# Optimization experiments

Measured on AMD Instinct MI355X. Metric: run time of the kernel, lower is better.

Reference implementation:

```python
import jax, jax.numpy as jnp
import numpy as np

M = 4096          # output features (n_rows, c_3)
H = 4096          # input features  (n_cols, c_4)
NNZ_PER_ROW = 2048
NNZ = M * NNZ_PER_ROW
B, S = 4, 2048    # batch, seq -> flattened to N = B*S row-vecs in the original loop


def setup_inputs() -> dict:
    key = jax.random.key(0)
    k1, k2, k3 = jax.random.split(key, 3)
    x = jax.random.normal(k1, (B, S, H), jnp.float32)
    values = jax.random.normal(k2, (NNZ,), jnp.float32) * 0.02
    # unique, sorted column indices per row (valid CSR structure)
    scores = jax.random.uniform(k3, (M, H))
    cols = jnp.argsort(scores, axis=1)[:, :NNZ_PER_ROW].astype(jnp.int32)
    col_idx = jnp.sort(cols, axis=1).reshape(-1)
    row_ptr = (jnp.arange(M + 1, dtype=jnp.int32) * NNZ_PER_ROW)
    return {"x": x, "values": values, "col_idx": col_idx, "row_ptr": row_ptr}


def _decode_csr(values, col_idx, row_ptr, n_rows, n_cols):
    """Decode compressed (CSR) weight once into dense [n_rows, n_cols]."""
    nnz = values.shape[0]
    row_ids = jnp.searchsorted(row_ptr, jnp.arange(nnz, dtype=row_ptr.dtype), side='right') - 1
    W = jnp.zeros((n_rows, n_cols), values.dtype).at[row_ids, col_idx].add(values)
    return W


def reference(x, values, col_idx, row_ptr):
    # Original loops macko_spmv.multiply over each flattened row of x:
    #   out_flat[i] = W_sparse @ x_flat[i]
    # Fused/batched equivalent: decode the compressed weight once, single GEMM.
    W = _decode_csr(values, col_idx, row_ptr, M, H)     # [M, H]
    out = jnp.einsum('bsh,mh->bsm', x, W)               # [B, S, M]
    return out
```

## Files before the change

### kernel.cpp

```cpp
#include <hip/hip_runtime.h>
#include <hip/hip_bf16.h>

#define H_DIM   4096
#define M_DIM   4096
#define N_ROWS  8192
#define NNZ_ROW 2048

typedef __bf16 bf16x8 __attribute__((ext_vector_type(8)));
typedef float  f32x4  __attribute__((ext_vector_type(4)));

__device__ __forceinline__ unsigned short f2bf(float f) {
    unsigned int u = __float_as_uint(f);
    u += 0x7fffu + ((u >> 16) & 1u);
    return (unsigned short)(u >> 16);
}

__device__ __forceinline__ void gld_lds16(const void* g, void* l) {
    __builtin_amdgcn_global_load_lds(
        (__attribute__((address_space(1))) const void*)g,
        (__attribute__((address_space(3))) void*)l,
        16, 0, 0);
}

__global__ __launch_bounds__(256) void decode_w_frag_kernel(
        const float* __restrict__ values,
        const int*   __restrict__ col_idx,
        unsigned short* __restrict__ Wf) {
    __shared__ unsigned short buf[4 * H_DIM];
    const int r4 = blockIdx.x;
    const int t  = threadIdx.x;

    uint4 z = make_uint4(0u, 0u, 0u, 0u);
    #pragma unroll
    for (int i = 0; i < 8; ++i) ((uint4*)buf)[i * 256 + t] = z;
    __syncthreads();

    #pragma unroll
    for (int rl = 0; rl < 4; ++rl) {
        const long base = ((long)(4 * r4 + rl)) * NNZ_ROW;
        #pragma unroll
        for (int j = 0; j < NNZ_ROW; j += 256) {
            float v = values[base + j + t];
            int   c = col_idx[base + j + t];
            buf[rl * H_DIM + c] = f2bf(v);
        }
    }
    __syncthreads();

    const int ct  = r4 >> 2;
    const int fr0 = (r4 & 3) * 4;
    #pragma unroll
    for (int it = 0; it < 8; ++it) {
        const int task = it * 256 + t;
        const int rl = task & 3;
        const int jq = (task >> 2) & 3;
        const int kc = task >> 4;
        uint4 v = *(const uint4*)&buf[rl * H_DIM + kc * 32 + jq * 8];
        const long dst = (((long)ct * 128 + kc) * 64 + jq * 16 + fr0 + rl) * 8;
        *(uint4*)&Wf[dst] = v;
    }
}

__global__ __launch_bounds__(256) void convert_x_kernel(
        const float4* __restrict__ x, uint4* __restrict__ xb) {
    const long i = blockIdx.x * 256L + threadIdx.x;
    float4 a = x[2 * i];
    float4 b = x[2 * i + 1];
    union { unsigned short s[8]; uint4 v; } r;
    r.s[0] = f2bf(a.x); r.s[1] = f2bf(a.y); r.s[2] = f2bf(a.z); r.s[3] = f2bf(a.w);
    r.s[4] = f2bf(b.x); r.s[5] = f2bf(b.y); r.s[6] = f2bf(b.z); r.s[7] = f2bf(b.w);
    xb[i] = r.v;
}

__global__ __launch_bounds__(256) void gemm_flatb_kernel(
        const unsigned short* __restrict__ A,
        const unsigned short* __restrict__ Bf,
        float* __restrict__ C) {
    __shared__ unsigned short As[128 * 32];

    const int t    = threadIdx.x;
    const int lane = t & 63;
    const int wid  = t >> 6;
    const int wm   = wid >> 1;
    const int wn   = wid & 1;

    const int gid   = blockIdx.x;
    const int ctile = (gid & 7) * 4 + ((gid >> 3) & 3);
    const int rtile = gid >> 5;
    const long row0 = (long)rtile * 128;
    const long col0 = (long)ctile * 128;

    const int ar = t >> 2;
    const int q  = t & 3;
    const unsigned short* Ag0 = A + (row0 + ar) * H_DIM + ((q ^ (ar & 3)) * 8);
    const unsigned short* Ag1 = Ag0 + 64L * H_DIM;
    unsigned short* Al0 = &As[t * 8];
    unsigned short* Al1 = &As[t * 8 + 2048];

    const uint4* Bbase = (const uint4*)Bf +
        ((long)(ctile * 8 + wn * 4) * 128) * 64 + lane;

    f32x4 acc[4][4];
    #pragma unroll
    for (int i = 0; i < 4; ++i)
        #pragma unroll
        for (int j = 0; j < 4; ++j)
            acc[i][j] = (f32x4)0.0f;

    const int fr = lane & 15;
    const int jq = lane >> 4;
    const int achunk = (jq ^ (fr & 3)) * 8;

    for (int kc = 0; kc < H_DIM / 32; ++kc) {
        __syncthreads();
        gld_lds16(Ag0 + kc * 32, Al0);
        gld_lds16(Ag1 + kc * 32, Al1);

        union { uint4 u; bf16x8 v; } b[4];
        #pragma unroll
        for (int j = 0; j < 4; ++j)
            b[j].u = Bbase[(long)kc * 64 + j * 128 * 64];

        __syncthreads();

        bf16x8 a[4];
        #pragma unroll
        for (int i = 0; i < 4; ++i) {
            const int r = wm * 64 + i * 16 + fr;
            a[i] = *(const bf16x8*)&As[r * 32 + achunk];
        }

        #pragma unroll
        for (int i = 0; i < 4; ++i)
            #pragma unroll
            for (int j = 0; j < 4; ++j)
                acc[i][j] = __builtin_amdgcn_mfma_f32_16x16x32_bf16(
                                a[i], b[j].v, acc[i][j], 0, 0, 0);
    }

    const int dcol = lane & 15;
    const int drow = (lane >> 4) * 4;
    #pragma unroll
    for (int i = 0; i < 4; ++i) {
        const long r = row0 + wm * 64 + i * 16 + drow;
        #pragma unroll
        for (int j = 0; j < 4; ++j) {
            float* cp = C + r * M_DIM + (col0 + wn * 64 + j * 16 + dcol);
            #pragma unroll
            for (int qq = 0; qq < 4; ++qq)
                cp[qq * (long)M_DIM] = acc[i][j][qq];
        }
    }
}

__global__ __launch_bounds__(256) void naive_kernel(
        const float* __restrict__ x, const float* __restrict__ vals,
        const int* __restrict__ cols, float* __restrict__ out) {
    const long idx = blockIdx.x * 256L + threadIdx.x;
    const int  m   = (int)(idx & (M_DIM - 1));
    const long n   = idx >> 12;
    const float* xr = x + n * H_DIM;
    const float* v  = vals + (long)m * NNZ_ROW;
    const int*   c  = cols + (long)m * NNZ_ROW;
    float s = 0.f;
    for (int j = 0; j < NNZ_ROW; ++j) s += v[j] * xr[c[j]];
    out[idx] = s;
}

extern "C" void kernel_launch(void* const* d_in, const int* in_sizes, int n_in,
                              void* d_out, int out_size, void* d_ws, size_t ws_size,
                              hipStream_t stream) {
    const float* x       = (const float*)d_in[0];
    const float* values  = (const float*)d_in[1];
    const int*   col_idx = (const int*)d_in[2];
    float* out = (float*)d_out;

    const size_t wbytes = (size_t)M_DIM * H_DIM * sizeof(unsigned short);
    const size_t xbytes = (size_t)N_ROWS * H_DIM * sizeof(unsigned short);

    if (ws_size >= wbytes + xbytes) {
        unsigned short* Wf = (unsigned short*)d_ws;
        unsigned short* Xb = (unsigned short*)((char*)d_ws + wbytes);

        decode_w_frag_kernel<<<M_DIM / 4, 256, 0, stream>>>(values, col_idx, Wf);

        const long xvec = (long)N_ROWS * H_DIM / 8;
        convert_x_kernel<<<(int)(xvec / 256), 256, 0, stream>>>(
            (const float4*)x, (uint4*)Xb);

        gemm_flatb_kernel<<<(N_ROWS / 128) * (M_DIM / 128), 256, 0, stream>>>(
            Xb, Wf, out);
    } else {
        naive_kernel<<<(int)((long)N_ROWS * M_DIM / 256), 256, 0, stream>>>(
            x, values, col_idx, out);
    }
}
```

Baseline: 616.3 us.

## Replace GEMM with 256x256 double-buffered LDS-tiled kernel and row-major W

The GEMM moves from 128x128 tiles, where B fragments come straight from global memory in a pre-shuffled layout, to 256x256 tiles with 8 waves. Both A and B are staged into double-buffered, XOR-swizzled LDS with global_load_lds, and explicit vmcnt/lgkmcnt waits, sched barriers and setprio interleave the loads with MFMA work. The W decode now writes plain row-major bf16, and the x conversion becomes a grid-stride loop. The aim is more data reuse per tile and hiding memory latency behind compute, at the cost of much more LDS per block (128 KB) and hand-tuned waitcnt logic that is fragile.

Result: faster. 499.5 us (-19.0%).

```diff
diff --git a/kernel.cpp b/kernel.cpp
--- a/kernel.cpp
+++ b/kernel.cpp
@@ -1,10 +1,10 @@
 #include <hip/hip_runtime.h>
-#include <hip/hip_bf16.h>
 
 #define H_DIM   4096
 #define M_DIM   4096
 #define N_ROWS  8192
 #define NNZ_ROW 2048
+#define NT      (H_DIM / 64)
 
 typedef __bf16 bf16x8 __attribute__((ext_vector_type(8)));
 typedef float  f32x4  __attribute__((ext_vector_type(4)));
@@ -22,10 +22,23 @@
         16, 0, 0);
 }
 
-__global__ __launch_bounds__(256) void decode_w_frag_kernel(
+__device__ __forceinline__ void wg_barrier() {
+    __builtin_amdgcn_sched_barrier(0);
+    asm volatile("" ::: "memory");
+    __builtin_amdgcn_s_barrier();
+    asm volatile("" ::: "memory");
+    __builtin_amdgcn_sched_barrier(0);
+}
+
+#define LGKM0_FENCE() do { \
+    asm volatile("s_waitcnt lgkmcnt(0)" ::: "memory"); \
+    __builtin_amdgcn_sched_barrier(0); \
+} while (0)
+
+__global__ __launch_bounds__(256) void decode_w_kernel(
         const float* __restrict__ values,
         const int*   __restrict__ col_idx,
-        unsigned short* __restrict__ Wf) {
+        unsigned short* __restrict__ W) {
     __shared__ unsigned short buf[4 * H_DIM];
     const int r4 = blockIdx.x;
     const int t  = threadIdx.x;
@@ -47,109 +60,188 @@
     }
     __syncthreads();
 
-    const int ct  = r4 >> 2;
-    const int fr0 = (r4 & 3) * 4;
+    const long wbase = (long)(4 * r4) * H_DIM;
     #pragma unroll
     for (int it = 0; it < 8; ++it) {
-        const int task = it * 256 + t;
-        const int rl = task & 3;
-        const int jq = (task >> 2) & 3;
-        const int kc = task >> 4;
-        uint4 v = *(const uint4*)&buf[rl * H_DIM + kc * 32 + jq * 8];
-        const long dst = (((long)ct * 128 + kc) * 64 + jq * 16 + fr0 + rl) * 8;
-        *(uint4*)&Wf[dst] = v;
+        const int s = it * 256 + t;
+        *(uint4*)&W[wbase + (long)s * 8] = *(const uint4*)&buf[s * 8];
     }
 }
 
 __global__ __launch_bounds__(256) void convert_x_kernel(
-        const float4* __restrict__ x, uint4* __restrict__ xb) {
-    const long i = blockIdx.x * 256L + threadIdx.x;
-    float4 a = x[2 * i];
-    float4 b = x[2 * i + 1];
-    union { unsigned short s[8]; uint4 v; } r;
-    r.s[0] = f2bf(a.x); r.s[1] = f2bf(a.y); r.s[2] = f2bf(a.z); r.s[3] = f2bf(a.w);
-    r.s[4] = f2bf(b.x); r.s[5] = f2bf(b.y); r.s[6] = f2bf(b.z); r.s[7] = f2bf(b.w);
-    xb[i] = r.v;
-}
-
-__global__ __launch_bounds__(256) void gemm_flatb_kernel(
+        const float4* __restrict__ x, unsigned long long* __restrict__ xb) {
+    const long total = (long)N_ROWS * H_DIM / 4;
+    for (long i = (long)blockIdx.x * 256 + threadIdx.x; i < total;
+         i += (long)gridDim.x * 256) {
+        float4 a = x[i];
+        union { unsigned short s[4]; unsigned long long v; } r;
+        r.s[0] = f2bf(a.x); r.s[1] = f2bf(a.y);
+        r.s[2] = f2bf(a.z); r.s[3] = f2bf(a.w);
+        xb[i] = r.v;
+    }
+}
+
+__global__ __launch_bounds__(512, 2) void gemm256_kernel(
         const unsigned short* __restrict__ A,
-        const unsigned short* __restrict__ Bf,
+        const unsigned short* __restrict__ B,
         float* __restrict__ C) {
-    __shared__ unsigned short As[128 * 32];
+    __shared__ unsigned short lds[2 * 32768];
 
     const int t    = threadIdx.x;
     const int lane = t & 63;
     const int wid  = t >> 6;
-    const int wm   = wid >> 1;
-    const int wn   = wid & 1;
-
-    const int gid   = blockIdx.x;
-    const int ctile = (gid & 7) * 4 + ((gid >> 3) & 3);
-    const int rtile = gid >> 5;
-    const long row0 = (long)rtile * 128;
-    const long col0 = (long)ctile * 128;
-
-    const int ar = t >> 2;
-    const int q  = t & 3;
-    const unsigned short* Ag0 = A + (row0 + ar) * H_DIM + ((q ^ (ar & 3)) * 8);
-    const unsigned short* Ag1 = Ag0 + 64L * H_DIM;
-    unsigned short* Al0 = &As[t * 8];
-    unsigned short* Al1 = &As[t * 8 + 2048];
-
-    const uint4* Bbase = (const uint4*)Bf +
-        ((long)(ctile * 8 + wn * 4) * 128) * 64 + lane;
-
-    f32x4 acc[4][4];
-    #pragma unroll
-    for (int i = 0; i < 4; ++i)
-        #pragma unroll
-        for (int j = 0; j < 4; ++j)
-            acc[i][j] = (f32x4)0.0f;
+    const int wm   = wid >> 2;
+    const int wn   = wid & 3;
+
+    const int bid   = blockIdx.x;
+    const int wg    = (bid & 7) * 64 + (bid >> 3);
+    const int ctile = wg >> 5;
+    const int rtile = wg & 31;
+    const long row0 = (long)rtile * 256;
+    const long col0 = (long)ctile * 256;
+
+    const int rr = t >> 3;
+    const int cc = ((t & 7) ^ (rr & 7)) * 8;
+    const unsigned short* pA = A + (row0 + rr) * H_DIM + cc;
+    const unsigned short* pB = B + (col0 + rr) * H_DIM + cc;
+    unsigned short* const Ld = &lds[t * 8];
+
+#define STAGE(bufo) do { \
+    gld_lds16(pA,               Ld + (bufo));         \
+    gld_lds16(pA +  64 * H_DIM, Ld + (bufo) + 4096);  \
+    gld_lds16(pA + 128 * H_DIM, Ld + (bufo) + 8192);  \
+    gld_lds16(pA + 192 * H_DIM, Ld + (bufo) + 12288); \
+    gld_lds16(pB,               Ld + (bufo) + 16384); \
+    gld_lds16(pB +  64 * H_DIM, Ld + (bufo) + 20480); \
+    gld_lds16(pB + 128 * H_DIM, Ld + (bufo) + 24576); \
+    gld_lds16(pB + 192 * H_DIM, Ld + (bufo) + 28672); \
+    pA += 64; pB += 64; \
+} while (0)
 
     const int fr = lane & 15;
     const int jq = lane >> 4;
-    const int achunk = (jq ^ (fr & 3)) * 8;
-
-    for (int kc = 0; kc < H_DIM / 32; ++kc) {
-        __syncthreads();
-        gld_lds16(Ag0 + kc * 32, Al0);
-        gld_lds16(Ag1 + kc * 32, Al1);
-
-        union { uint4 u; bf16x8 v; } b[4];
+    const int cx = fr & 7;
+    const int off0 = ((0 * 4 + jq) ^ cx) * 8;
+    const int off1 = ((1 * 4 + jq) ^ cx) * 8;
+    const int aoff = wm * 8192 + fr * 64;
+    const int boff = 16384 + (wn >> 1) * 8192 + ((wn & 1) * 64 + fr) * 64;
+
+    f32x4 acc[8][4];
+    #pragma unroll
+    for (int i = 0; i < 8; ++i)
+        #pragma unroll
+        for (int j = 0; j < 4; ++j) acc[i][j] = (f32x4)0.0f;
+
+    auto TILE = [&](const int cb) {
+        const unsigned short* Ab = &lds[cb + aoff];
+        const unsigned short* Bb = &lds[cb + boff];
+        bf16x8 a[4][2], b0[2][2], b1[2][2];
+        #pragma unroll
+        for (int i = 0; i < 4; ++i) {
+            a[i][0] = *(const bf16x8*)(Ab + i * 1024 + off0);
+            a[i][1] = *(const bf16x8*)(Ab + i * 1024 + off1);
+        }
+        #pragma unroll
+        for (int j = 0; j < 2; ++j) {
+            b0[j][0] = *(const bf16x8*)(Bb + j * 1024 + off0);
+            b0[j][1] = *(const bf16x8*)(Bb + j * 1024 + off1);
+        }
+        LGKM0_FENCE();
+        __builtin_amdgcn_s_setprio(1);
+        #pragma unroll
+        for (int i = 0; i < 4; ++i)
+            #pragma unroll
+            for (int j = 0; j < 2; ++j) {
+                acc[i][j] = __builtin_amdgcn_mfma_f32_16x16x32_bf16(
+                                a[i][0], b0[j][0], acc[i][j], 0, 0, 0);
+                acc[i][j] = __builtin_amdgcn_mfma_f32_16x16x32_bf16(
+                                a[i][1], b0[j][1], acc[i][j], 0, 0, 0);
+            }
+        __builtin_amdgcn_s_setprio(0);
+        #pragma unroll
+        for (int j = 0; j < 2; ++j) {
+            b1[j][0] = *(const bf16x8*)(Bb + (2 + j) * 1024 + off0);
+            b1[j][1] = *(const bf16x8*)(Bb + (2 + j) * 1024 + off1);
+        }
+        LGKM0_FENCE();
+        __builtin_amdgcn_s_setprio(1);
+        #pragma unroll
+        for (int i = 0; i < 4; ++i)
+            #pragma unroll
+            for (int j = 0; j < 2; ++j) {
+                acc[i][2 + j] = __builtin_amdgcn_mfma_f32_16x16x32_bf16(
+                                    a[i][0], b1[j][0], acc[i][2 + j], 0, 0, 0);
+                acc[i][2 + j] = __builtin_amdgcn_mfma_f32_16x16x32_bf16(
+                                    a[i][1], b1[j][1], acc[i][2 + j], 0, 0, 0);
+            }
+        __builtin_amdgcn_s_setprio(0);
+        #pragma unroll
+        for (int i = 0; i < 4; ++i) {
+            a[i][0] = *(const bf16x8*)(Ab + (4 + i) * 1024 + off0);
+            a[i][1] = *(const bf16x8*)(Ab + (4 + i) * 1024 + off1);
+        }
+        LGKM0_FENCE();
+        __builtin_amdgcn_s_setprio(1);
+        #pragma unroll
+        for (int i = 0; i < 4; ++i)
+            #pragma unroll
+            for (int j = 0; j < 2; ++j) {
+                acc[4 + i][2 + j] = __builtin_amdgcn_mfma_f32_16x16x32_bf16(
+                                        a[i][0], b1[j][0], acc[4 + i][2 + j], 0, 0, 0);
+                acc[4 + i][2 + j] = __builtin_amdgcn_mfma_f32_16x16x32_bf16(
+                                        a[i][1], b1[j][1], acc[4 + i][2 + j], 0, 0, 0);
+            }
+        __builtin_amdgcn_s_setprio(0);
+        __builtin_amdgcn_s_setprio(1);
+        #pragma unroll
+        for (int i = 0; i < 4; ++i)
+            #pragma unroll
+            for (int j = 0; j < 2; ++j) {
+                acc[4 + i][j] = __builtin_amdgcn_mfma_f32_16x16x32_bf16(
+                                    a[i][0], b0[j][0], acc[4 + i][j], 0, 0, 0);
+                acc[4 + i][j] = __builtin_amdgcn_mfma_f32_16x16x32_bf16(
+                                    a[i][1], b0[j][1], acc[4 + i][j], 0, 0, 0);
+            }
+        __builtin_amdgcn_s_setprio(0);
+    };
+
+    STAGE(0);
+    #pragma unroll 1
+    for (int kt = 0; kt < NT - 2; kt += 2) {
+        STAGE(32768);
+        asm volatile("s_waitcnt vmcnt(8)" ::: "memory");
+        wg_barrier();
+        TILE(0);
+        wg_barrier();
+        STAGE(0);
+        asm volatile("s_waitcnt vmcnt(8)" ::: "memory");
+        wg_barrier();
+        TILE(32768);
+        wg_barrier();
+    }
+    STAGE(32768);
+    asm volatile("s_waitcnt vmcnt(8)" ::: "memory");
+    wg_barrier();
+    TILE(0);
+    wg_barrier();
+    asm volatile("s_waitcnt vmcnt(0)" ::: "memory");
+    wg_barrier();
+    TILE(32768);
+
+#undef STAGE
+
+    const int dcol = lane & 15;
+    const int dr4  = (lane >> 4) * 4;
+    const long crow = row0 + wm * 128;
+    const int  ccol = (int)col0 + wn * 64 + dcol;
+    #pragma unroll
+    for (int i = 0; i < 8; ++i) {
+        float* cp = C + (crow + i * 16 + dr4) * M_DIM + ccol;
         #pragma unroll
         for (int j = 0; j < 4; ++j)
-            b[j].u = Bbase[(long)kc * 64 + j * 128 * 64];
-
-        __syncthreads();
-
-        bf16x8 a[4];
-        #pragma unroll
-        for (int i = 0; i < 4; ++i) {
-            const int r = wm * 64 + i * 16 + fr;
-            a[i] = *(const bf16x8*)&As[r * 32 + achunk];
-        }
-
-        #pragma unroll
-        for (int i = 0; i < 4; ++i)
-            #pragma unroll
-            for (int j = 0; j < 4; ++j)
-                acc[i][j] = __builtin_amdgcn_mfma_f32_16x16x32_bf16(
-                                a[i], b[j].v, acc[i][j], 0, 0, 0);
-    }
-
-    const int dcol = lane & 15;
-    const int drow = (lane >> 4) * 4;
-    #pragma unroll
-    for (int i = 0; i < 4; ++i) {
-        const long r = row0 + wm * 64 + i * 16 + drow;
-        #pragma unroll
-        for (int j = 0; j < 4; ++j) {
-            float* cp = C + r * M_DIM + (col0 + wn * 64 + j * 16 + dcol);
-            #pragma unroll
-            for (int qq = 0; qq < 4; ++qq)
-                cp[qq * (long)M_DIM] = acc[i][j][qq];
-        }
+            #pragma unroll
+            for (int q = 0; q < 4; ++q)
+                cp[(long)q * M_DIM + j * 16] = acc[i][j][q];
     }
 }
 
@@ -179,17 +271,13 @@
     const size_t xbytes = (size_t)N_ROWS * H_DIM * sizeof(unsigned short);
 
     if (ws_size >= wbytes + xbytes) {
-        unsigned short* Wf = (unsigned short*)d_ws;
+        unsigned short* Wd = (unsigned short*)d_ws;
         unsigned short* Xb = (unsigned short*)((char*)d_ws + wbytes);
 
-        decode_w_frag_kernel<<<M_DIM / 4, 256, 0, stream>>>(values, col_idx, Wf);
-
-        const long xvec = (long)N_ROWS * H_DIM / 8;
-        convert_x_kernel<<<(int)(xvec / 256), 256, 0, stream>>>(
-            (const float4*)x, (uint4*)Xb);
-
-        gemm_flatb_kernel<<<(N_ROWS / 128) * (M_DIM / 128), 256, 0, stream>>>(
-            Xb, Wf, out);
+        decode_w_kernel<<<M_DIM / 4, 256, 0, stream>>>(values, col_idx, Wd);
+        convert_x_kernel<<<4096, 256, 0, stream>>>(
+            (const float4*)x, (unsigned long long*)Xb);
+        gemm256_kernel<<<512, 512, 0, stream>>>(Xb, Wd, out);
     } else {
         naive_kernel<<<(int)((long)N_ROWS * M_DIM / 256), 256, 0, stream>>>(
             x, values, col_idx, out);
```
